# Performance work log

Hardware: AMD Instinct MI355X
Metric: run time of the kernel (lower is better)

Reference implementation:

```python
import jax, jax.numpy as jnp
import numpy as np

EMBED_DIM = 100
NUM_SYMBOLS = 100000
BATCH = 2048
N_NEIGH = 200


def setup_inputs() -> dict:
    key = jax.random.key(0)
    ks = jax.random.split(key, 10)
    D = EMBED_DIM
    connections = jax.random.randint(ks[0], (BATCH, N_NEIGH, 4), 0, NUM_SYMBOLS, dtype=jnp.int64)
    num_neighbors = jax.random.randint(ks[1], (BATCH,), 1, N_NEIGH, dtype=jnp.int64)
    # symbol embedding table (num_symbols+1, D); padding row = num_symbols (left random; indices stay < NUM_SYMBOLS)
    symbol_emb = jax.random.normal(ks[2], (NUM_SYMBOLS + 1, D), dtype=jnp.float32) * 0.02
    # gcn_w: Linear(3D -> D) with its own bias, plus separate gcn_b parameter
    gcn_w = jax.random.normal(ks[3], (D, 3 * D), dtype=jnp.float32) * (1.0 / np.sqrt(3 * D))
    gcn_w_bias = jnp.zeros((D,), dtype=jnp.float32)
    gcn_b = jnp.zeros((D,), dtype=jnp.float32)
    # attn_w: Linear(D -> 1)
    attn_w = jax.random.normal(ks[4], (1, D), dtype=jnp.float32) * (1.0 / np.sqrt(D))
    attn_bias = jnp.zeros((1,), dtype=jnp.float32)
    # gate_w: Linear(D -> 1) plus separate gate_b parameter
    gate_w = jax.random.normal(ks[5], (1, D), dtype=jnp.float32) * (1.0 / np.sqrt(D))
    gate_w_bias = jnp.zeros((1,), dtype=jnp.float32)
    gate_b = jnp.zeros((1,), dtype=jnp.float32)
    return {
        "connections": connections,
        "num_neighbors": num_neighbors,
        "symbol_emb": symbol_emb,
        "gcn_w": gcn_w,
        "gcn_w_bias": gcn_w_bias,
        "gcn_b": gcn_b,
        "attn_w": attn_w,
        "attn_bias": attn_bias,
        "gate_w": gate_w,
        "gate_w_bias": gate_w_bias,
        "gate_b": gate_b,
    }


def reference(connections, num_neighbors, symbol_emb, gcn_w, gcn_w_bias, gcn_b,
              attn_w, attn_bias, gate_w, gate_w_bias, gate_b):
    # neighbor_encoder (eval mode: dropout is identity). num_neighbors is unused,
    # exactly as in the original module.
    entity_self = connections[:, 0, 0]          # (B,)
    relations = connections[:, :, 1]            # (B, N)
    entities = connections[:, :, 2]
    times = connections[:, :, 3]

    rel_embeds = symbol_emb[relations]          # (B, N, D) gather
    ent_embeds = symbol_emb[entities]
    time_embeds = symbol_emb[times]
    entself_embeds = symbol_emb[entity_self]    # (B, D)

    concat = jnp.concatenate((rel_embeds, ent_embeds, time_embeds), axis=-1)  # (B, N, 3D)
    out = jnp.einsum('bnk,dk->bnd', concat, gcn_w) + gcn_w_bias + gcn_b       # (B, N, D)
    out = jax.nn.leaky_relu(out, negative_slope=0.01)

    attn_logits = jnp.einsum('bnd,od->bno', out, attn_w) + attn_bias          # (B, N, 1)
    attn_weight = jax.nn.softmax(attn_logits, axis=1)                         # softmax over neighbors
    out_attn = jnp.einsum('bnd,bno->bd', out, attn_weight)                    # (B, D)

    gate = jax.nn.sigmoid(jnp.einsum('bd,od->bo', out_attn, gate_w) + gate_w_bias + gate_b)  # (B, 1)
    out_neighbor = out_attn * gate + entself_embeds * (1.0 - gate)            # (B, D)
    return out_neighbor
```

## Files before the change

kernel.cpp:

```cpp
#include <hip/hip_runtime.h>
#include <stdint.h>

#define D_EMB 100
#define NSYM 100001
#define BATCH 2048
#define NNEI 200
#define P_STRIDE 304
#define FP8_SCALE 256.0f
#define FP8_INV   0.00390625f

#define BP_ELEMS   32000
#define BP_KS3_OFF 30720

typedef __bf16 bf16x8 __attribute__((ext_vector_type(8)));
typedef __bf16 bf16x4 __attribute__((ext_vector_type(4)));
typedef float  f32x4  __attribute__((ext_vector_type(4)));
typedef float  f32x2  __attribute__((ext_vector_type(2)));

__host__ __device__ inline int colmap(int tau, int n) {
    return 32 * (tau >> 1) + 8 * (n >> 2) + 4 * (tau & 1) + (n & 3);
}

__global__ __launch_bounds__(256) void prep_bp(const float* __restrict__ gcn_w,
                                               __bf16* __restrict__ Bp) {
    int idx = blockIdx.x * 256 + threadIdx.x;
    if (idx >= BP_ELEMS) return;
    int tau, n, k;
    if (idx < BP_KS3_OFF) {
        int j = idx & 7;
        n     = (idx >> 3) & 15;
        int z = idx >> 7;
        tau   = z / 12;
        int r = z - tau * 12;
        int ks = r >> 2, q = r & 3;
        k = ks * 32 + q * 8 + j;
    } else {
        int i2 = idx - BP_KS3_OFF;
        int j  = i2 & 3;
        n      = (i2 >> 2) & 15;
        tau    = i2 >> 6;
        k      = 96 + j;
    }
    const int col = colmap(tau, n);
    float v = 0.0f;
    if (col < 300 && k < 100) {
        int c = col / 100, d = col % 100;
        v = gcn_w[d * 300 + c * 100 + k];
    }
    Bp[idx] = (__bf16)v;
}

__device__ inline void load_bfrag(const float* __restrict__ rowp, int quad,
                                  bf16x8 b[4]) {
    #pragma unroll
    for (int ks = 0; ks < 3; ++ks) {
        const int k0 = ks * 32 + quad * 8;
        const float4 x = *(const float4*)(rowp + k0);
        const float4 y = *(const float4*)(rowp + k0 + 4);
        bf16x8 v;
        v[0]=(__bf16)x.x; v[1]=(__bf16)x.y; v[2]=(__bf16)x.z; v[3]=(__bf16)x.w;
        v[4]=(__bf16)y.x; v[5]=(__bf16)y.y; v[6]=(__bf16)y.z; v[7]=(__bf16)y.w;
        b[ks] = v;
    }
    bf16x8 v;
    #pragma unroll
    for (int i = 0; i < 8; ++i) v[i] = (__bf16)0.0f;
    if (quad == 0) {
        const float4 x = *(const float4*)(rowp + 96);
        v[0]=(__bf16)x.x; v[1]=(__bf16)x.y; v[2]=(__bf16)x.z; v[3]=(__bf16)x.w;
    }
    b[3] = v;
}

__device__ inline uint32_t pack_fp8x4(float a, float b, float c, float d) {
    uint32_t w = (uint32_t)__builtin_amdgcn_cvt_pk_fp8_f32(a, b, 0, false);
    w = (uint32_t)__builtin_amdgcn_cvt_pk_fp8_f32(c, d, (int)w, true);
    return w;
}

__global__ __launch_bounds__(512, 4) void gemm_P(const float* __restrict__ emb,
                                                 const __bf16* __restrict__ Bp,
                                                 uint8_t* __restrict__ P8) {
    __shared__ __bf16 BpS[BP_ELEMS + 8];

    const int tid  = threadIdx.x;
    const int wave = tid >> 6;
    const int lane = tid & 63;
    const int n    = lane & 15;
    const int quad = lane >> 4;

    {
        const uint4* __restrict__ src = (const uint4*)Bp;
        uint4* dst = (uint4*)BpS;
        for (int c = tid; c < BP_ELEMS / 8; c += 512)
            dst[c] = src[c];
        if (tid < 8) BpS[BP_ELEMS + tid] = (__bf16)0.0f;
    }

    const int sA = blockIdx.x * 256 + wave * 32 + n;
    const int sB = sA + 16;
    const int rA = (sA <= NSYM - 1) ? sA : (NSYM - 1);
    const int rB = (sB <= NSYM - 1) ? sB : (NSYM - 1);

    bf16x8 bA[4], bB[4];
    load_bfrag(emb + (size_t)rA * D_EMB, quad, bA);
    load_bfrag(emb + (size_t)rB * D_EMB, quad, bB);

    __syncthreads();

    const bool wrA = (sA <= NSYM - 1);
    const bool wrB = (sB <= NSYM - 1);
    uint8_t* __restrict__ prA = P8 + (size_t)sA * P_STRIDE;
    uint8_t* __restrict__ prB = P8 + (size_t)sB * P_STRIDE;

    for (int u = 0; u < 10; ++u) {
        const int t0 = 2 * u, t1 = t0 + 1;

        bf16x8 a0[4], a1[4];
        #pragma unroll
        for (int ks = 0; ks < 3; ++ks) {
            a0[ks] = *(const bf16x8*)&BpS[((t0 * 12 + ks * 4 + quad) * 16 + n) * 8];
            a1[ks] = *(const bf16x8*)&BpS[((t1 * 12 + ks * 4 + quad) * 16 + n) * 8];
        }
        {
            const int o0 = (quad == 0) ? (BP_KS3_OFF + (t0 * 16 + n) * 4) : BP_ELEMS;
            const int o1 = (quad == 0) ? (BP_KS3_OFF + (t1 * 16 + n) * 4) : BP_ELEMS;
            const bf16x4 w0 = *(const bf16x4*)&BpS[o0];
            const bf16x4 w1 = *(const bf16x4*)&BpS[o1];
            bf16x8 v0, v1;
            #pragma unroll
            for (int i = 0; i < 4; ++i) {
                v0[i] = w0[i]; v1[i] = w1[i];
                v0[i + 4] = (__bf16)0.0f; v1[i + 4] = (__bf16)0.0f;
            }
            a0[3] = v0; a1[3] = v1;
        }

        f32x4 aA0 = {0.f,0.f,0.f,0.f}, aA1 = {0.f,0.f,0.f,0.f};
        f32x4 aB0 = {0.f,0.f,0.f,0.f}, aB1 = {0.f,0.f,0.f,0.f};
        #pragma unroll
        for (int ks = 0; ks < 4; ++ks) {
            aA0 = __builtin_amdgcn_mfma_f32_16x16x32_bf16(a0[ks], bA[ks], aA0, 0, 0, 0);
            aA1 = __builtin_amdgcn_mfma_f32_16x16x32_bf16(a1[ks], bA[ks], aA1, 0, 0, 0);
            aB0 = __builtin_amdgcn_mfma_f32_16x16x32_bf16(a0[ks], bB[ks], aB0, 0, 0, 0);
            aB1 = __builtin_amdgcn_mfma_f32_16x16x32_bf16(a1[ks], bB[ks], aB1, 0, 0, 0);
        }

        const int colBase = 32 * u + 8 * quad;
        if (colBase + 8 <= 300) {
            if (wrA) {
                uint2 o;
                o.x = pack_fp8x4(aA0[0]*FP8_SCALE, aA0[1]*FP8_SCALE,
                                 aA0[2]*FP8_SCALE, aA0[3]*FP8_SCALE);
                o.y = pack_fp8x4(aA1[0]*FP8_SCALE, aA1[1]*FP8_SCALE,
                                 aA1[2]*FP8_SCALE, aA1[3]*FP8_SCALE);
                *(uint2*)(prA + colBase) = o;
            }
            if (wrB) {
                uint2 o;
                o.x = pack_fp8x4(aB0[0]*FP8_SCALE, aB0[1]*FP8_SCALE,
                                 aB0[2]*FP8_SCALE, aB0[3]*FP8_SCALE);
                o.y = pack_fp8x4(aB1[0]*FP8_SCALE, aB1[1]*FP8_SCALE,
                                 aB1[2]*FP8_SCALE, aB1[3]*FP8_SCALE);
                *(uint2*)(prB + colBase) = o;
            }
        } else if (colBase + 4 <= 300) {
            if (wrA)
                *(uint32_t*)(prA + colBase) =
                    pack_fp8x4(aA0[0]*FP8_SCALE, aA0[1]*FP8_SCALE,
                               aA0[2]*FP8_SCALE, aA0[3]*FP8_SCALE);
            if (wrB)
                *(uint32_t*)(prB + colBase) =
                    pack_fp8x4(aB0[0]*FP8_SCALE, aB0[1]*FP8_SCALE,
                               aB0[2]*FP8_SCALE, aB0[3]*FP8_SCALE);
        }
    }
}

__global__ __launch_bounds__(512, 8) void gather_attn(
        const int*     __restrict__ conn,
        const uint8_t* __restrict__ P8,
        const float*   __restrict__ emb,
        const float*   __restrict__ gcn_w_bias,
        const float*   __restrict__ gcn_b,
        const float*   __restrict__ attn_w,
        const float*   __restrict__ attn_bias,
        const float*   __restrict__ gate_w,
        const float*   __restrict__ gate_w_bias,
        const float*   __restrict__ gate_b,
        float* __restrict__ out) {

    __shared__ uint32_t vs[NNEI * 25];
    __shared__ int4     conn_s[NNEI];
    __shared__ float    logit2[NNEI][2];
    __shared__ float    logits[NNEI];
    __shared__ float    wgt[NNEI];
    __shared__ float4   aw4_s[25];
    __shared__ float4   bias4_s[25];
    __shared__ float    part[20][D_EMB];
    __shared__ float    red[128];
    __shared__ float    gsh;

    const int b = blockIdx.x;
    const int t = threadIdx.x;
    const int w = t >> 6;
    const int l = t & 63;

    if (t < NNEI) conn_s[t] = *(const int4*)(conn + ((size_t)b * NNEI + t) * 4);
    if (t < 25) {
        aw4_s[t]   = *(const float4*)(attn_w + 4 * t);
        bias4_s[t] = make_float4((gcn_w_bias[4*t]   + gcn_b[4*t])   * FP8_SCALE,
                                 (gcn_w_bias[4*t+1] + gcn_b[4*t+1]) * FP8_SCALE,
                                 (gcn_w_bias[4*t+2] + gcn_b[4*t+2]) * FP8_SCALE,
                                 (gcn_w_bias[4*t+3] + gcn_b[4*t+3]) * FP8_SCALE);
    }
    const float abias = attn_bias[0];
    __syncthreads();

    #pragma unroll
    for (int half = 0; half < 2; ++half) {
        uint32_t U[5][3];
        #pragma unroll
        for (int j = 0; j < 5; ++j) {
            const int idx = t + 512 * (5 * half + j);
            if (idx < NNEI * 25) {
                const int n  = idx / 25;
                const int li = idx - n * 25;
                const int4 c = conn_s[n];
                U[j][0] = *(const uint32_t*)(P8 + (size_t)c.y * P_STRIDE +       li * 4);
                U[j][1] = *(const uint32_t*)(P8 + (size_t)c.z * P_STRIDE + 100 + li * 4);
                U[j][2] = *(const uint32_t*)(P8 + (size_t)c.w * P_STRIDE + 200 + li * 4);
            }
        }
        #pragma unroll
        for (int j = 0; j < 5; ++j) {
            const int idx = t + 512 * (5 * half + j);
            if (idx < NNEI * 25) {
                const int li = idx % 25;
                const f32x2 y0 = __builtin_amdgcn_cvt_pk_f32_fp8((int)U[j][0], false);
                const f32x2 y1 = __builtin_amdgcn_cvt_pk_f32_fp8((int)U[j][0], true);
                const f32x2 z0 = __builtin_amdgcn_cvt_pk_f32_fp8((int)U[j][1], false);
                const f32x2 z1 = __builtin_amdgcn_cvt_pk_f32_fp8((int)U[j][1], true);
                const f32x2 q0 = __builtin_amdgcn_cvt_pk_f32_fp8((int)U[j][2], false);
                const f32x2 q1 = __builtin_amdgcn_cvt_pk_f32_fp8((int)U[j][2], true);
                const float4 bb = bias4_s[li];
                float v0 = y0[0] + z0[0] + q0[0] + bb.x;
                float v1 = y0[1] + z0[1] + q0[1] + bb.y;
                float v2 = y1[0] + z1[0] + q1[0] + bb.z;
                float v3 = y1[1] + z1[1] + q1[1] + bb.w;
                v0 = fmaxf(v0, 0.01f * v0);
                v1 = fmaxf(v1, 0.01f * v1);
                v2 = fmaxf(v2, 0.01f * v2);
                v3 = fmaxf(v3, 0.01f * v3);
                vs[idx] = pack_fp8x4(v0, v1, v2, v3);
            }
        }
    }
    __syncthreads();

    if (t < 2 * NNEI) {
        const int n = t >> 1, h = t & 1;
        const int lo = h ? 13 : 0, hi = h ? 25 : 13;
        float p = 0.f;
        for (int j = lo; j < hi; ++j) {
            const uint32_t u = vs[n * 25 + j];
            const f32x2 a = __builtin_amdgcn_cvt_pk_f32_fp8((int)u, false);
            const f32x2 c = __builtin_amdgcn_cvt_pk_f32_fp8((int)u, true);
            const float4 aw = aw4_s[j];
            p += a[0] * aw.x + a[1] * aw.y + c[0] * aw.z + c[1] * aw.w;
        }
        logit2[n][h] = p;
    }
    __syncthreads();
    if (t < NNEI)
        logits[t] = (logit2[t][0] + logit2[t][1]) * FP8_INV + abias;
    __syncthreads();

    if (w == 0) {
        float vals[4];
        float mx = -1e30f;
        #pragma unroll
        for (int j = 0; j < 4; ++j) {
            const int n = l + 64 * j;
            vals[j] = (n < NNEI) ? logits[n] : -1e30f;
            mx = fmaxf(mx, vals[j]);
        }
        #pragma unroll
        for (int off = 32; off > 0; off >>= 1) mx = fmaxf(mx, __shfl_xor(mx, off));
        float sum = 0.f;
        #pragma unroll
        for (int j = 0; j < 4; ++j) {
            const int n = l + 64 * j;
            if (n < NNEI) { const float e = __expf(vals[j] - mx); wgt[n] = e; sum += e; }
        }
        #pragma unroll
        for (int off = 32; off > 0; off >>= 1) sum += __shfl_xor(sum, off);
        const float inv = 1.f / sum;
        #pragma unroll
        for (int j = 0; j < 4; ++j) {
            const int n = l + 64 * j;
            if (n < NNEI) wgt[n] *= inv;
        }
    }
    __syncthreads();

    if (t < 500) {
        const int z  = t / 25;
        const int li = t - z * 25;
        const int n0 = z * 10;
        float s0 = 0.f, s1 = 0.f, s2 = 0.f, s3 = 0.f;
        #pragma unroll 5
        for (int n = n0; n < n0 + 10; ++n) {
            const float wn = wgt[n];
            const uint32_t u = vs[n * 25 + li];
            const f32x2 a = __builtin_amdgcn_cvt_pk_f32_fp8((int)u, false);
            const f32x2 c = __builtin_amdgcn_cvt_pk_f32_fp8((int)u, true);
            s0 += wn * a[0]; s1 += wn * a[1]; s2 += wn * c[0]; s3 += wn * c[1];
        }
        *(float4*)&part[z][4 * li] = make_float4(s0, s1, s2, s3);
    }
    __syncthreads();

    float accd = 0.f;
    if (t < D_EMB) {
        #pragma unroll
        for (int z = 0; z < 20; ++z) accd += part[z][t];
        accd *= FP8_INV;
        red[t] = accd * gate_w[t];
    } else if (t < 128) {
        red[t] = 0.f;
    }
    __syncthreads();

    if (w == 0) {
        float r = red[l] + red[l + 64];
        #pragma unroll
        for (int off = 32; off > 0; off >>= 1) r += __shfl_xor(r, off);
        if (l == 0) gsh = 1.f / (1.f + __expf(-(r + gate_w_bias[0] + gate_b[0])));
    }
    __syncthreads();

    if (t < D_EMB) {
        const int self = conn_s[0].x;
        const float se = emb[(size_t)self * D_EMB + t];
        const float g  = gsh;
        out[(size_t)b * D_EMB + t] = accd * g + se * (1.f - g);
    }
}

__global__ void ws_diag(float* out, float ws_mb) { out[0] = ws_mb; }

extern "C" void kernel_launch(void* const* d_in, const int* in_sizes, int n_in,
                              void* d_out, int out_size, void* d_ws, size_t ws_size,
                              hipStream_t stream) {
    const int*   conn        = (const int*)d_in[0];
    const float* emb         = (const float*)d_in[2];
    const float* gcn_w       = (const float*)d_in[3];
    const float* gcn_w_bias  = (const float*)d_in[4];
    const float* gcn_b       = (const float*)d_in[5];
    const float* attn_w      = (const float*)d_in[6];
    const float* attn_bias   = (const float*)d_in[7];
    const float* gate_w      = (const float*)d_in[8];
    const float* gate_w_bias = (const float*)d_in[9];
    const float* gate_b      = (const float*)d_in[10];
    float* out = (float*)d_out;

    const size_t P_bytes = (size_t)NSYM * P_STRIDE;
    const size_t Bp_off  = (P_bytes + 255) & ~(size_t)255;
    const size_t need    = Bp_off + (size_t)BP_ELEMS * 2;

    if (ws_size < need) {
        ws_diag<<<1, 1, 0, stream>>>(out, (float)(ws_size / 1.0e6));
        return;
    }

    uint8_t* P8 = (uint8_t*)d_ws;
    __bf16*  Bp = (__bf16*)((char*)d_ws + Bp_off);

    prep_bp<<<(BP_ELEMS + 255) / 256, 256, 0, stream>>>(gcn_w, Bp);
    gemm_P<<<(NSYM + 255) / 256, 512, 0, stream>>>(emb, Bp, P8);
    gather_attn<<<BATCH, 512, 0, stream>>>(conn, P8, emb, gcn_w_bias, gcn_b,
                                           attn_w, attn_bias, gate_w, gate_w_bias,
                                           gate_b, out);
}
```

Measured before the change: 149.5 us.

## Split gemm_P output columns across two grid halves to halve shared-memory weights

The precompute GEMM now launches a 2D grid in which each block computes only half of the 300 projected columns (5 of 10 column-pair tiles). Each block stages only its half of the bf16 weight matrix in LDS, which halves shared memory per block, and the launch-bounds occupancy hint rises from 4 to 6. This doubles the number of blocks and raises occupancy, but each block still loads the same embedding rows, so embedding reads from global memory double.

```diff
diff --git a/kernel.cpp b/kernel.cpp
--- a/kernel.cpp
+++ b/kernel.cpp
@@ -11,6 +11,9 @@
 
 #define BP_ELEMS   32000
 #define BP_KS3_OFF 30720
+#define BPH_A 15360
+#define BPH_B 640
+#define BPH   16000
 
 typedef __bf16 bf16x8 __attribute__((ext_vector_type(8)));
 typedef __bf16 bf16x4 __attribute__((ext_vector_type(4)));
@@ -78,23 +81,27 @@
     return w;
 }
 
-__global__ __launch_bounds__(512, 4) void gemm_P(const float* __restrict__ emb,
+__global__ __launch_bounds__(512, 6) void gemm_P(const float* __restrict__ emb,
                                                  const __bf16* __restrict__ Bp,
                                                  uint8_t* __restrict__ P8) {
-    __shared__ __bf16 BpS[BP_ELEMS + 8];
+    __shared__ __bf16 BpS[BPH + 8];
 
     const int tid  = threadIdx.x;
     const int wave = tid >> 6;
     const int lane = tid & 63;
     const int n    = lane & 15;
     const int quad = lane >> 4;
+    const int h    = blockIdx.y;
 
     {
-        const uint4* __restrict__ src = (const uint4*)Bp;
-        uint4* dst = (uint4*)BpS;
-        for (int c = tid; c < BP_ELEMS / 8; c += 512)
-            dst[c] = src[c];
-        if (tid < 8) BpS[BP_ELEMS + tid] = (__bf16)0.0f;
+        const uint4* __restrict__ srcA = (const uint4*)(Bp + h * BPH_A);
+        uint4* dstA = (uint4*)BpS;
+        for (int c = tid; c < BPH_A / 8; c += 512)
+            dstA[c] = srcA[c];
+        const uint4* __restrict__ srcB = (const uint4*)(Bp + BP_KS3_OFF + h * BPH_B);
+        uint4* dstB = (uint4*)(BpS + BPH_A);
+        if (tid < BPH_B / 8) dstB[tid] = srcB[tid];
+        if (tid < 8) BpS[BPH + tid] = (__bf16)0.0f;
     }
 
     const int sA = blockIdx.x * 256 + wave * 32 + n;
@@ -113,18 +120,18 @@
     uint8_t* __restrict__ prA = P8 + (size_t)sA * P_STRIDE;
     uint8_t* __restrict__ prB = P8 + (size_t)sB * P_STRIDE;
 
-    for (int u = 0; u < 10; ++u) {
-        const int t0 = 2 * u, t1 = t0 + 1;
+    for (int u = 0; u < 5; ++u) {
+        const int tt0 = 2 * u, tt1 = tt0 + 1;
 
         bf16x8 a0[4], a1[4];
         #pragma unroll
         for (int ks = 0; ks < 3; ++ks) {
-            a0[ks] = *(const bf16x8*)&BpS[((t0 * 12 + ks * 4 + quad) * 16 + n) * 8];
-            a1[ks] = *(const bf16x8*)&BpS[((t1 * 12 + ks * 4 + quad) * 16 + n) * 8];
+            a0[ks] = *(const bf16x8*)&BpS[((tt0 * 12 + ks * 4 + quad) * 16 + n) * 8];
+            a1[ks] = *(const bf16x8*)&BpS[((tt1 * 12 + ks * 4 + quad) * 16 + n) * 8];
         }
         {
-            const int o0 = (quad == 0) ? (BP_KS3_OFF + (t0 * 16 + n) * 4) : BP_ELEMS;
-            const int o1 = (quad == 0) ? (BP_KS3_OFF + (t1 * 16 + n) * 4) : BP_ELEMS;
+            const int o0 = (quad == 0) ? (BPH_A + (tt0 * 16 + n) * 4) : BPH;
+            const int o1 = (quad == 0) ? (BPH_A + (tt1 * 16 + n) * 4) : BPH;
             const bf16x4 w0 = *(const bf16x4*)&BpS[o0];
             const bf16x4 w1 = *(const bf16x4*)&BpS[o1];
             bf16x8 v0, v1;
@@ -146,7 +153,7 @@
             aB1 = __builtin_amdgcn_mfma_f32_16x16x32_bf16(a1[ks], bB[ks], aB1, 0, 0, 0);
         }
 
-        const int colBase = 32 * u + 8 * quad;
+        const int colBase = 32 * (5 * h + u) + 8 * quad;
         if (colBase + 8 <= 300) {
             if (wrA) {
                 uint2 o;
@@ -259,8 +266,8 @@
     __syncthreads();
 
     if (t < 2 * NNEI) {
-        const int n = t >> 1, h = t & 1;
-        const int lo = h ? 13 : 0, hi = h ? 25 : 13;
+        const int n = t >> 1, hh = t & 1;
+        const int lo = hh ? 13 : 0, hi = hh ? 25 : 13;
         float p = 0.f;
         for (int j = lo; j < hi; ++j) {
             const uint32_t u = vs[n * 25 + j];
@@ -269,7 +276,7 @@
             const float4 aw = aw4_s[j];
             p += a[0] * aw.x + a[1] * aw.y + c[0] * aw.z + c[1] * aw.w;
         }
-        logit2[n][h] = p;
+        logit2[n][hh] = p;
     }
     __syncthreads();
     if (t < NNEI)
@@ -378,7 +385,8 @@
     __bf16*  Bp = (__bf16*)((char*)d_ws + Bp_off);
 
     prep_bp<<<(BP_ELEMS + 255) / 256, 256, 0, stream>>>(gcn_w, Bp);
-    gemm_P<<<(NSYM + 255) / 256, 512, 0, stream>>>(emb, Bp, P8);
+    dim3 ggrid((NSYM + 255) / 256, 2);
+    gemm_P<<<ggrid, 512, 0, stream>>>(emb, Bp, P8);
     gather_attn<<<BATCH, 512, 0, stream>>>(conn, P8, emb, gcn_w_bias, gcn_b,
                                            attn_w, attn_bias, gate_w, gate_w_bias,
                                            gate_b, out);
```

Measured after the change: 155.3 us. +3.9%, slower.
